# Optimization experiments

Hardware: AMD Instinct MI355X
Metric: run time of the kernel (lower is better)

Reference implementation:

```python
import jax, jax.numpy as jnp
import numpy as np

N_NODES = 100000
NEG_SLOPE = 0.2


def leaky_relu(x):
    return jnp.where(x >= 0, x, NEG_SLOPE * x)


def gat_conv(x, src, dst, W, a_src, a_dst, b, heads, out_ch, concat):
    # x: [N, F_in]; src/dst: [E]; W: [F_in, heads*out_ch]
    n = x.shape[0]
    h = (x @ W).reshape(n, heads, out_ch)                      # [N, H, C]
    s_src = jnp.einsum('nhc,hc->nh', h, a_src)                 # [N, H]
    s_dst = jnp.einsum('nhc,hc->nh', h, a_dst)                 # [N, H]
    e = leaky_relu(s_src[src] + s_dst[dst])                    # [E, H]
    # segment softmax over incoming edges of each dst node
    m = jax.ops.segment_max(e, dst, num_segments=n)            # [N, H]
    m = jnp.where(jnp.isfinite(m), m, 0.0)
    p = jnp.exp(e - m[dst])                                    # [E, H]
    denom = jax.ops.segment_sum(p, dst, num_segments=n)        # [N, H]
    alpha = p / denom[dst]                                     # [E, H]
    out = jax.ops.segment_sum(h[src] * alpha[..., None], dst, num_segments=n)  # [N, H, C]
    if concat:
        out = out.reshape(n, heads * out_ch)
    else:
        out = out.mean(axis=1)
    return out + b


def setup_inputs() -> dict:
    key = jax.random.key(0)
    ks = jax.random.split(key, 10)
    F_in, hidden, heads, n_cls = 128, 32, 8, 40
    n_edges = 1600000
    x = jax.random.normal(ks[0], (N_NODES, F_in), dtype=jnp.float32)
    edge_index = jax.random.randint(ks[1], (2, n_edges), 0, N_NODES, dtype=jnp.int64)
    s = 0.1
    W1 = jax.random.normal(ks[2], (F_in, heads * hidden), dtype=jnp.float32) * s
    att_src1 = jax.random.normal(ks[3], (heads, hidden), dtype=jnp.float32) * s
    att_dst1 = jax.random.normal(ks[4], (heads, hidden), dtype=jnp.float32) * s
    b1 = jnp.zeros((heads * hidden,), dtype=jnp.float32)
    W2 = jax.random.normal(ks[5], (heads * hidden, n_cls), dtype=jnp.float32) * s
    att_src2 = jax.random.normal(ks[6], (1, n_cls), dtype=jnp.float32) * s
    att_dst2 = jax.random.normal(ks[7], (1, n_cls), dtype=jnp.float32) * s
    b2 = jnp.zeros((n_cls,), dtype=jnp.float32)
    return {
        'x': x, 'edge_index': edge_index,
        'W1': W1, 'att_src1': att_src1, 'att_dst1': att_dst1, 'b1': b1,
        'W2': W2, 'att_src2': att_src2, 'att_dst2': att_dst2, 'b2': b2,
    }


def reference(x, edge_index, W1, att_src1, att_dst1, b1, W2, att_src2, att_dst2, b2):
    n = x.shape[0]
    # PyG GATConv default: add self loops
    loop = jnp.arange(n, dtype=edge_index.dtype)
    src = jnp.concatenate([edge_index[0], loop])
    dst = jnp.concatenate([edge_index[1], loop])
    h = gat_conv(x, src, dst, W1, att_src1, att_dst1, b1, heads=8, out_ch=32, concat=True)
    h = jax.nn.relu(h)  # dropout p=0 / eval mode: identity
    out = gat_conv(h, src, dst, W2, att_src2, att_dst2, b2, heads=1, out_ch=40, concat=True)
    return jax.nn.log_softmax(out, axis=1)
```

## Files before the change

### kernel.cpp

```cpp
#include <hip/hip_runtime.h>
#include <hip/hip_bf16.h>
#include <cmath>


typedef unsigned short ushortT;
typedef unsigned int uintT;
typedef unsigned char ucharT;
typedef __attribute__((ext_vector_type(8))) short short8;
typedef __attribute__((ext_vector_type(4))) float float4v;
typedef __attribute__((ext_vector_type(2))) float float2v;

#define LOG2E 1.4426950408889634f

static __device__ __forceinline__ float bflo(uintT u) {
    return __uint_as_float(u << 16);
}
static __device__ __forceinline__ float bfhi(uintT u) {
    return __uint_as_float(u & 0xffff0000u);
}
static __device__ __forceinline__ ushortT f2bf(float f) {
    __hip_bfloat16 h = __float2bfloat16(f);
    return *reinterpret_cast<ushortT*>(&h);
}
static __device__ __forceinline__ uintT pk(float a, float b) {
    return (uintT)f2bf(a) | ((uintT)f2bf(b) << 16);
}
static __device__ __forceinline__ float ub(uintT u, int k) {
    return (float)((u >> (8 * k)) & 0xffu);
}
static __device__ __forceinline__ float lrelu(float e) {
    return 0.6f * e + 0.4f * fabsf(e);
}

#define PREP_BLOCKS 184
#define EPB 4096

__global__ __launch_bounds__(256) void k_prep(const float* __restrict__ W1,
                                              const float* __restrict__ W2,
                                              const float* __restrict__ a1s,
                                              const float* __restrict__ a1d,
                                              ushortT* __restrict__ W1t,
                                              ushortT* __restrict__ W2t) {
    int t = blockIdx.x * 256 + threadIdx.x;
    if (t < 128 * 256) {
        int k = t >> 8, s = t & 255;
        int c = ((s & 15) << 4) | (s >> 4);
        W1t[s * 128 + k] = f2bf(W1[(size_t)k * 256 + c]);
    } else if (t < 128 * 256 + 48 * 256) {
        int q = t - 128 * 256;
        int k = q / 48, c = q - k * 48;
        W2t[c * 256 + k] = (c < 40) ? f2bf(W2[k * 40 + c]) : (ushortT)0;
    } else if (t < 128 * 256 + 48 * 256 + 2048) {
        int q = t - (128 * 256 + 48 * 256);
        int k = q >> 4, j = q & 15;
        int h = j & 7;
        const float* av = ((j < 8) ? a1s : a1d) + h * 32;
        const float* wr = W1 + (size_t)k * 256 + h * 32;
        float s = 0.f;
        #pragma unroll
        for (int c = 0; c < 32; ++c) s += wr[c] * av[c];
        W1t[(256 + j) * 128 + k] = f2bf(s * LOG2E);
    }
}

static __device__ __forceinline__ void dev_gemm1(int slab,
                                                 const float* __restrict__ A,
                                                 const ushortT* __restrict__ Bt,
                                                 ucharT* __restrict__ h1i,
                                                 float* __restrict__ s1cc,
                                                 float* __restrict__ s1d, int M) {
    int lane = threadIdx.x & 63;
    int r0 = slab * 16;
    if (r0 >= M) return;
    int n = lane & 15, q = lane >> 4;
    const float* arow = A + (size_t)(r0 + n) * 128 + q * 8;
    short8 af[4];
    #pragma unroll
    for (int s = 0; s < 4; ++s) {
        float4 v0 = *(const float4*)(arow + s * 32);
        float4 v1 = *(const float4*)(arow + s * 32 + 4);
        short8 a;
        a[0] = (short)f2bf(v0.x); a[1] = (short)f2bf(v0.y);
        a[2] = (short)f2bf(v0.z); a[3] = (short)f2bf(v0.w);
        a[4] = (short)f2bf(v1.x); a[5] = (short)f2bf(v1.y);
        a[6] = (short)f2bf(v1.z); a[7] = (short)f2bf(v1.w);
        af[s] = a;
    }
    float4v acc[17];
    #pragma unroll
    for (int j = 0; j < 17; ++j) acc[j] = (float4v){0.f, 0.f, 0.f, 0.f};
    #pragma unroll
    for (int s = 0; s < 4; ++s) {
        #pragma unroll
        for (int j = 0; j < 17; ++j) {
            short8 b = *(const short8*)(Bt + (size_t)(j * 16 + n) * 128 + s * 32 + q * 8);
            acc[j] = __builtin_amdgcn_mfma_f32_16x16x32_bf16(af[s], b, acc[j], 0, 0, 0);
        }
    }
    float am[4];
    #pragma unroll
    for (int r = 0; r < 4; ++r) {
        float m = 0.f;
        #pragma unroll
        for (int j = 0; j < 16; ++j) m = fmaxf(m, fabsf(acc[j][r]));
        am[r] = m;
    }
    #pragma unroll
    for (int off = 1; off < 16; off <<= 1) {
        #pragma unroll
        for (int r = 0; r < 4; ++r) am[r] = fmaxf(am[r], __shfl_xor(am[r], off, 64));
    }
    #pragma unroll
    for (int r = 0; r < 4; ++r) {
        int row = r0 + q * 4 + r;
        float m = am[r];
        float si = (m > 0.f) ? 127.f / m : 0.f;
        uintT wd[4];
        #pragma unroll
        for (int wq = 0; wq < 4; ++wq) {
            uintT p4 = 0;
            #pragma unroll
            for (int b = 0; b < 4; ++b) {
                int j = wq * 4 + b;
                int qv = (int)rintf(acc[j][r] * si) + 128;
                p4 |= ((uintT)(qv & 0xff)) << (8 * b);
            }
            wd[wq] = p4;
        }
        uint4 o = make_uint4(wd[0], wd[1], wd[2], wd[3]);
        *(uint4*)(h1i + (size_t)row * 256 + n * 16) = o;
        float vv = acc[16][r];
        if (n < 8) {
            *(float2*)(s1cc + ((size_t)row << 4) + n * 2) =
                make_float2(vv, m * (1.f / 127.f));
        } else {
            s1d[(size_t)row * 8 + (n - 8)] = vv;
        }
    }
}

__global__ __launch_bounds__(256) void k_cnt_g1(const int* __restrict__ ei, int E,
                                                int* __restrict__ counts, int nbuck,
                                                const float* __restrict__ A,
                                                const ushortT* __restrict__ Bt,
                                                ucharT* __restrict__ h1i,
                                                float* __restrict__ s1cc,
                                                float* __restrict__ s1d,
                                                int M, int nPrim, int slabBase) {
    if (blockIdx.x >= nPrim) {
        int wave = threadIdx.x >> 6;
        int slab = slabBase + (blockIdx.x - nPrim) * 4 + wave;
        dev_gemm1(slab, A, Bt, h1i, s1cc, s1d, M);
        return;
    }
    __shared__ int h[1024];
    int t = threadIdx.x;
    for (int i = t; i < nbuck; i += 256) h[i] = 0;
    __syncthreads();
    int base = blockIdx.x * EPB;
    #pragma unroll
    for (int r = 0; r < 4; ++r) {
        int i4 = base + (r * 256 + t) * 4;
        if (i4 + 3 < E) {
            int4 d = *(const int4*)(ei + E + i4);
            atomicAdd(&h[d.x >> 7], 1);
            atomicAdd(&h[d.y >> 7], 1);
            atomicAdd(&h[d.z >> 7], 1);
            atomicAdd(&h[d.w >> 7], 1);
        } else {
            for (int j = i4; j < E; ++j) atomicAdd(&h[ei[E + j] >> 7], 1);
        }
    }
    __syncthreads();
    int* crow = counts + (size_t)blockIdx.x * nbuck;
    for (int i = t; i < nbuck; i += 256) crow[i] = h[i];
}

__global__ __launch_bounds__(256) void k_scan_cols(int* __restrict__ counts,
                                                   int* __restrict__ totals,
                                                   int nb1, int nbuck) {
    __shared__ int wsum[4];
    int k = blockIdx.x;
    int t = threadIdx.x, lane = t & 63, wv = t >> 6;
    int e0 = 2 * t, e1 = 2 * t + 1;
    int v0 = (e0 < nb1) ? counts[(size_t)e0 * nbuck + k] : 0;
    int v1 = (e1 < nb1) ? counts[(size_t)e1 * nbuck + k] : 0;
    int s = v0 + v1;
    int incl = s;
    #pragma unroll
    for (int off = 1; off < 64; off <<= 1) {
        int u = __shfl_up(incl, off, 64);
        if (lane >= off) incl += u;
    }
    if (lane == 63) wsum[wv] = incl;
    __syncthreads();
    int add = 0;
    if (wv > 0) add += wsum[0];
    if (wv > 1) add += wsum[1];
    if (wv > 2) add += wsum[2];
    incl += add;
    int excl = incl - s;
    if (e0 < nb1) counts[(size_t)e0 * nbuck + k] = excl;
    if (e1 < nb1) counts[(size_t)e1 * nbuck + k] = excl + v0;
    if (t == 255) totals[k] = incl;
}

__global__ __launch_bounds__(256) void k_place_g1(const int* __restrict__ ei, int E,
                                                  const int* __restrict__ counts,
                                                  const int* __restrict__ totals,
                                                  int* __restrict__ bstart,
                                                  uintT* __restrict__ tmp, int nbuck,
                                                  const float* __restrict__ A,
                                                  const ushortT* __restrict__ Bt,
                                                  ucharT* __restrict__ h1i,
                                                  float* __restrict__ s1cc,
                                                  float* __restrict__ s1d,
                                                  int M, int nPrim, int slabBase) {
    if (blockIdx.x >= nPrim) {
        int wave = threadIdx.x >> 6;
        int slab = slabBase + (blockIdx.x - nPrim) * 4 + wave;
        dev_gemm1(slab, A, Bt, h1i, s1cc, s1d, M);
        return;
    }
    __shared__ int st[1024];
    __shared__ int pos[1024];
    __shared__ int wsum[4];
    int t = threadIdx.x, lane = t & 63, wv = t >> 6;
    int b = blockIdx.x;
    int g[4];
    int s = 0;
    #pragma unroll
    for (int j = 0; j < 4; ++j) {
        int e = 4 * t + j;
        g[j] = (e < nbuck) ? totals[e] : 0;
        s += g[j];
    }
    int incl = s;
    #pragma unroll
    for (int off = 1; off < 64; off <<= 1) {
        int u = __shfl_up(incl, off, 64);
        if (lane >= off) incl += u;
    }
    if (lane == 63) wsum[wv] = incl;
    __syncthreads();
    int add = 0;
    if (wv > 0) add += wsum[0];
    if (wv > 1) add += wsum[1];
    if (wv > 2) add += wsum[2];
    int excl = incl + add - s;
    #pragma unroll
    for (int j = 0; j < 4; ++j) {
        int e = 4 * t + j;
        if (e < nbuck) st[e] = excl;
        excl += g[j];
    }
    __syncthreads();
    const int* crow = counts + (size_t)b * nbuck;
    for (int i = t; i < nbuck; i += 256) {
        int sv = st[i];
        pos[i] = sv + crow[i];
        if (b == 0) bstart[i] = sv;
    }
    __syncthreads();
    int base = b * EPB;
    #pragma unroll
    for (int r = 0; r < 4; ++r) {
        int i4 = base + (r * 256 + t) * 4;
        if (i4 + 3 < E) {
            int4 sv = *(const int4*)(ei + i4);
            int4 dv = *(const int4*)(ei + E + i4);
            int p0 = atomicAdd(&pos[dv.x >> 7], 1);
            tmp[p0] = (uintT)sv.x | (((uintT)dv.x & 127u) << 17);
            int p1 = atomicAdd(&pos[dv.y >> 7], 1);
            tmp[p1] = (uintT)sv.y | (((uintT)dv.y & 127u) << 17);
            int p2 = atomicAdd(&pos[dv.z >> 7], 1);
            tmp[p2] = (uintT)sv.z | (((uintT)dv.z & 127u) << 17);
            int p3 = atomicAdd(&pos[dv.w >> 7], 1);
            tmp[p3] = (uintT)sv.w | (((uintT)dv.w & 127u) << 17);
        } else {
            for (int j = i4; j < E; ++j) {
                int sj = ei[j], dj = ei[E + j];
                int p = atomicAdd(&pos[dj >> 7], 1);
                tmp[p] = (uintT)sj | (((uintT)dj & 127u) << 17);
            }
        }
    }
}

static __device__ __forceinline__ void dev_csr(int k,
                                               const uintT* __restrict__ tmp,
                                               const int* __restrict__ bstart,
                                               const int* __restrict__ totals,
                                               int* __restrict__ rowptr,
                                               int* __restrict__ csr_src,
                                               int N, int* cnt, int* cur,
                                               int* wtot) {
    int t = threadIdx.x;
    int nodeBase = k << 7;
    int nn = N - nodeBase;
    if (nn > 128) nn = 128;
    int myStart = bstart[k];
    int myCount = totals[k];
    int csrBase = myStart + nodeBase;
    if (t < 128) cnt[t] = 0;
    __syncthreads();
    for (int i = t; i < myCount; i += 256) {
        uintT p = tmp[myStart + i];
        atomicAdd(&cnt[p >> 17], 1);
    }
    __syncthreads();
    int dseg = 0, incl = 0;
    if (t < 128) {
        dseg = (t < nn) ? cnt[t] + 1 : 0;
        incl = dseg;
        #pragma unroll
        for (int off = 1; off < 64; off <<= 1) {
            int u = __shfl_up(incl, off, 64);
            if ((t & 63) >= off) incl += u;
        }
        if (t == 63) *wtot = incl;
    }
    __syncthreads();
    if (t < nn) {
        int excl = incl - dseg + ((t >= 64) ? *wtot : 0);
        int rp = csrBase + excl;
        int node = nodeBase + t;
        rowptr[node + 1] = rp + dseg;
        csr_src[rp] = node;
        cur[t] = rp + 1;
    }
    if (k == 0 && t == 0) rowptr[0] = 0;
    __syncthreads();
    for (int i = t; i < myCount; i += 256) {
        uintT p = tmp[myStart + i];
        int ld = p >> 17;
        int q = atomicAdd(&cur[ld], 1);
        csr_src[q] = (int)(p & 0x1FFFFu);
    }
}

__global__ __launch_bounds__(256) void k_csr_g1(const uintT* __restrict__ tmp,
                                                const int* __restrict__ bstart,
                                                const int* __restrict__ totals,
                                                int* __restrict__ rowptr,
                                                int* __restrict__ csr_src,
                                                int N,
                                                const float* __restrict__ A,
                                                const ushortT* __restrict__ Bt,
                                                ucharT* __restrict__ h1i,
                                                float* __restrict__ s1cc,
                                                float* __restrict__ s1d,
                                                int M, int nPrim, int slabBase) {
    __shared__ int cnt[128];
    __shared__ int cur[128];
    __shared__ int wtot;
    if (blockIdx.x >= nPrim) {
        int wave = threadIdx.x >> 6;
        int slab = slabBase + (blockIdx.x - nPrim) * 4 + wave;
        dev_gemm1(slab, A, Bt, h1i, s1cc, s1d, M);
        return;
    }
    dev_csr(blockIdx.x, tmp, bstart, totals, rowptr, csr_src, N, cnt, cur, &wtot);
}

struct Edge1 {
    float2 svc;
    uint4 v;
    int si;
};

static __device__ __forceinline__ void ldi1(Edge1& S, int j, int endm1,
                                            const int* __restrict__ csr_src) {
    int jj = j < endm1 ? j : endm1;
    S.si = csr_src[jj];
}

static __device__ __forceinline__ void ldv1(Edge1& S, int j, int end,
                                            const float2* __restrict__ sc2,
                                            const ucharT* __restrict__ hb, int head) {
    if (j < end) {
        int s = S.si;
        S.svc = sc2[((size_t)s << 3) + head];
        S.v = *(const uint4*)(hb + ((size_t)s << 8));
    }
}

static __device__ __forceinline__ void ac1(const Edge1& S, float sdn,
                                           float2v* A, float& l, float& sps) {
    float p = exp2f(lrelu(S.svc.x + sdn));
    l += p;
    float ps = p * S.svc.y;
    sps += ps;
    float2v p2 = {ps, ps};
    uintT w;
    w = S.v.x;
    A[0] += p2 * (float2v){ub(w, 0), ub(w, 1)};
    A[1] += p2 * (float2v){ub(w, 2), ub(w, 3)};
    w = S.v.y;
    A[2] += p2 * (float2v){ub(w, 0), ub(w, 1)};
    A[3] += p2 * (float2v){ub(w, 2), ub(w, 3)};
    w = S.v.z;
    A[4] += p2 * (float2v){ub(w, 0), ub(w, 1)};
    A[5] += p2 * (float2v){ub(w, 2), ub(w, 3)};
    w = S.v.w;
    A[6] += p2 * (float2v){ub(w, 0), ub(w, 1)};
    A[7] += p2 * (float2v){ub(w, 2), ub(w, 3)};
}

static __device__ __forceinline__ void dev_agg1(int n,
                                                const ucharT* __restrict__ h1i,
                                                const float* __restrict__ s1cc,
                                                const float* __restrict__ s1d,
                                                const int* __restrict__ rowptr,
                                                const int* __restrict__ csr_src,
                                                const float* __restrict__ b1,
                                                ushortT* __restrict__ out1) {
    int lane = threadIdx.x & 63;
    int g = lane >> 4;
    int cl = lane & 15;
    int head = cl >> 1;
    int beg = rowptr[n], end = rowptr[n + 1];
    float sdn = s1d[(size_t)n * 8 + head];
    const ucharT* hb = h1i + cl * 16;
    const float2* sc2 = (const float2*)s1cc;
    float2v A[8];
    #pragma unroll
    for (int k = 0; k < 8; ++k) A[k] = (float2v){0.f, 0.f};
    float l = 0.f, sps = 0.f;
    int i0 = beg + g;
    if (i0 < end) {
        int endm1 = end - 1;
        Edge1 S0, S1, S2;
        S0.svc = S1.svc = S2.svc = make_float2(0.f, 0.f);
        S0.v = S1.v = S2.v = make_uint4(0u, 0u, 0u, 0u);
        ldi1(S0, i0, endm1, csr_src);
        ldi1(S1, i0 + 4, endm1, csr_src);
        ldi1(S2, i0 + 8, endm1, csr_src);
        ldv1(S0, i0, end, sc2, hb, head);
        ldv1(S1, i0 + 4, end, sc2, hb, head);
        ldv1(S2, i0 + 8, end, sc2, hb, head);
        ldi1(S0, i0 + 12, endm1, csr_src);
        ldi1(S1, i0 + 16, endm1, csr_src);
        ldi1(S2, i0 + 20, endm1, csr_src);
        for (int idx = i0; idx < end; idx += 12) {
            ac1(S0, sdn, A, l, sps);
            ldv1(S0, idx + 12, end, sc2, hb, head);
            ldi1(S0, idx + 24, endm1, csr_src);
            if (idx + 4 < end) {
                ac1(S1, sdn, A, l, sps);
                ldv1(S1, idx + 16, end, sc2, hb, head);
                ldi1(S1, idx + 28, endm1, csr_src);
            }
            if (idx + 8 < end) {
                ac1(S2, sdn, A, l, sps);
                ldv1(S2, idx + 20, end, sc2, hb, head);
                ldi1(S2, idx + 32, endm1, csr_src);
            }
        }
    }
    #pragma unroll
    for (int off = 16; off < 64; off <<= 1) {
        l += __shfl_xor(l, off, 64);
        sps += __shfl_xor(sps, off, 64);
        #pragma unroll
        for (int k = 0; k < 8; ++k) {
            A[k].x += __shfl_xor(A[k].x, off, 64);
            A[k].y += __shfl_xor(A[k].y, off, 64);
        }
    }
    if (g == 0) {
        float inv = 1.f / l;
        float adj = 128.f * sps;
        const float4 bb0 = *(const float4*)(b1 + cl * 16);
        const float4 bb1 = *(const float4*)(b1 + cl * 16 + 4);
        const float4 bb2 = *(const float4*)(b1 + cl * 16 + 8);
        const float4 bb3 = *(const float4*)(b1 + cl * 16 + 12);
        float bbf[16] = {bb0.x, bb0.y, bb0.z, bb0.w, bb1.x, bb1.y, bb1.z, bb1.w,
                         bb2.x, bb2.y, bb2.z, bb2.w, bb3.x, bb3.y, bb3.z, bb3.w};
        uintT o[8];
        #pragma unroll
        for (int k = 0; k < 8; ++k) {
            float x0 = fmaxf((A[k].x - adj) * inv + bbf[2 * k], 0.f);
            float x1 = fmaxf((A[k].y - adj) * inv + bbf[2 * k + 1], 0.f);
            o[k] = pk(x0, x1);
        }
        *(uint4*)(out1 + (size_t)n * 256 + cl * 16) =
            make_uint4(o[0], o[1], o[2], o[3]);
        *(uint4*)(out1 + (size_t)n * 256 + cl * 16 + 8) =
            make_uint4(o[4], o[5], o[6], o[7]);
    }
}

__global__ __launch_bounds__(256) void k_csr_agg1(const uintT* __restrict__ tmp,
                                                  const int* __restrict__ bstart,
                                                  const int* __restrict__ totals,
                                                  int* __restrict__ rowptr,
                                                  int* __restrict__ csr_src,
                                                  int N, int halfB, int nP4,
                                                  const ucharT* __restrict__ h1i,
                                                  const float* __restrict__ s1cc,
                                                  const float* __restrict__ s1d,
                                                  const float* __restrict__ b1,
                                                  ushortT* __restrict__ out1, int H) {
    __shared__ int cnt[128];
    __shared__ int cur[128];
    __shared__ int wtot;
    if (blockIdx.x < nP4) {
        dev_csr(halfB + blockIdx.x, tmp, bstart, totals, rowptr, csr_src, N,
                cnt, cur, &wtot);
        return;
    }
    int n = (blockIdx.x - nP4) * 4 + (threadIdx.x >> 6);
    if (n >= H) return;
    dev_agg1(n, h1i, s1cc, s1d, rowptr, csr_src, b1, out1);
}

__global__ __launch_bounds__(256) void k_agg1(const ucharT* __restrict__ h1i,
                                              const float* __restrict__ s1cc,
                                              const float* __restrict__ s1d,
                                              const int* __restrict__ rowptr,
                                              const int* __restrict__ csr_src,
                                              const float* __restrict__ b1,
                                              ushortT* __restrict__ out1,
                                              int base, int N) {
    int n = base + blockIdx.x * 4 + (threadIdx.x >> 6);
    if (n >= N) return;
    dev_agg1(n, h1i, s1cc, s1d, rowptr, csr_src, b1, out1);
}

__global__ __launch_bounds__(256) void k_gemm2(const ushortT* __restrict__ X,
                                               const ushortT* __restrict__ Bt,
                                               const float* __restrict__ a2s,
                                               const float* __restrict__ a2d,
                                               ushortT* __restrict__ H2,
                                               float* __restrict__ s2d, int M) {
    int lane = threadIdx.x & 63, wave = threadIdx.x >> 6;
    int slab = blockIdx.x * 4 + wave;
    int r0 = slab * 16;
    if (r0 >= M) return;
    int n = lane & 15, q = lane >> 4;
    const ushortT* xrow = X + (size_t)(r0 + n) * 256 + q * 8;
    float4v acc[3];
    #pragma unroll
    for (int j = 0; j < 3; ++j) acc[j] = (float4v){0.f, 0.f, 0.f, 0.f};
    #pragma unroll
    for (int s = 0; s < 8; ++s) {
        short8 a = *(const short8*)(xrow + s * 32);
        #pragma unroll
        for (int j = 0; j < 3; ++j) {
            short8 b = *(const short8*)(Bt + (size_t)(j * 16 + n) * 256 + s * 32 + q * 8);
            acc[j] = __builtin_amdgcn_mfma_f32_16x16x32_bf16(a, b, acc[j], 0, 0, 0);
        }
    }
    float asv[3], adv[3];
    #pragma unroll
    for (int j = 0; j < 3; ++j) {
        int col = j * 16 + n;
        asv[j] = (col < 40) ? a2s[col] * LOG2E : 0.f;
        adv[j] = (col < 40) ? a2d[col] * LOG2E : 0.f;
    }
    float us[4], ud[4];
    #pragma unroll
    for (int r = 0; r < 4; ++r) {
        us[r] = acc[0][r] * asv[0] + acc[1][r] * asv[1] + acc[2][r] * asv[2];
        ud[r] = acc[0][r] * adv[0] + acc[1][r] * adv[1] + acc[2][r] * adv[2];
    }
    #pragma unroll
    for (int off = 1; off < 16; off <<= 1) {
        #pragma unroll
        for (int r = 0; r < 4; ++r) {
            us[r] += __shfl_xor(us[r], off, 64);
            ud[r] += __shfl_xor(ud[r], off, 64);
        }
    }
    #pragma unroll
    for (int j = 0; j < 3; ++j) {
        int col = j * 16 + n;
        if (col < 40) {
            #pragma unroll
            for (int r = 0; r < 4; ++r)
                H2[(size_t)(r0 + q * 4 + r) * 48 + col] = f2bf(acc[j][r]);
        }
    }
    if (n == 0) {
        #pragma unroll
        for (int r = 0; r < 4; ++r) {
            int row = r0 + q * 4 + r;
            *(float*)(H2 + (size_t)row * 48 + 40) = us[r];
            s2d[row] = ud[r];
        }
    }
}

struct Edge2 {
    float sv;
    uint2 v;
    int si;
};

static __device__ __forceinline__ void ldi2(Edge2& S, int j, int endm1,
                                            const int* __restrict__ csr_src) {
    int jj = j < endm1 ? j : endm1;
    S.si = csr_src[jj];
}

static __device__ __forceinline__ void ldv2(Edge2& S, int j, int end,
                                            const ushortT* __restrict__ h2, int cl) {
    if (j < end) {
        int s = S.si;
        const ushortT* hr = h2 + (size_t)s * 48;
        S.v = *(const uint2*)(hr + cl * 4);
        S.sv = *(const float*)(hr + 40);
    }
}

static __device__ __forceinline__ void ac2(const Edge2& S, float sdn,
                                           float2v& A01, float2v& A23, float& l) {
    float p = exp2f(lrelu(S.sv + sdn));
    l += p;
    float2v p2 = {p, p};
    A01 += p2 * (float2v){bflo(S.v.x), bfhi(S.v.x)};
    A23 += p2 * (float2v){bflo(S.v.y), bfhi(S.v.y)};
}

__global__ __launch_bounds__(256) void k_agg2lsm(const ushortT* __restrict__ h2,
                                                 const float* __restrict__ sd,
                                                 const int* __restrict__ rowptr,
                                                 const int* __restrict__ csr_src,
                                                 const float* __restrict__ b2,
                                                 float* __restrict__ out, int N) {
    int lane = threadIdx.x & 63;
    int wid = threadIdx.x >> 6;
    int n = blockIdx.x * 4 + wid;
    if (n >= N) return;
    int el = lane / 10;
    int cl = lane - el * 10;
    int beg = rowptr[n], end = rowptr[n + 1];
    float sdn = sd[n];
    float2v A01 = (float2v){0.f, 0.f}, A23 = (float2v){0.f, 0.f};
    float l = 0.f;
    if (el < 6) {
        int i0 = beg + el;
        if (i0 < end) {
            int endm1 = end - 1;
            Edge2 S0, S1, S2;
            S0.sv = S1.sv = S2.sv = 0.f;
            S0.v = S1.v = S2.v = make_uint2(0u, 0u);
            ldi2(S0, i0, endm1, csr_src);
            ldi2(S1, i0 + 6, endm1, csr_src);
            ldi2(S2, i0 + 12, endm1, csr_src);
            ldv2(S0, i0, end, h2, cl);
            ldv2(S1, i0 + 6, end, h2, cl);
            ldv2(S2, i0 + 12, end, h2, cl);
            ldi2(S0, i0 + 18, endm1, csr_src);
            ldi2(S1, i0 + 24, endm1, csr_src);
            ldi2(S2, i0 + 30, endm1, csr_src);
            for (int idx = i0; idx < end; idx += 18) {
                ac2(S0, sdn, A01, A23, l);
                ldv2(S0, idx + 18, end, h2, cl);
                ldi2(S0, idx + 36, endm1, csr_src);
                if (idx + 6 < end) {
                    ac2(S1, sdn, A01, A23, l);
                    ldv2(S1, idx + 24, end, h2, cl);
                    ldi2(S1, idx + 42, endm1, csr_src);
                }
                if (idx + 12 < end) {
                    ac2(S2, sdn, A01, A23, l);
                    ldv2(S2, idx + 30, end, h2, cl);
                    ldi2(S2, idx + 48, endm1, csr_src);
                }
            }
        }
    }
    float a0 = A01.x, a1 = A01.y, a2 = A23.x, a3 = A23.y;
    float t0 = 0.f, t1 = 0.f, t2 = 0.f, t3 = 0.f, lt = 0.f;
    #pragma unroll
    for (int k = 0; k < 6; ++k) {
        int sl = cl + 10 * k;
        t0 += __shfl(a0, sl, 64);
        t1 += __shfl(a1, sl, 64);
        t2 += __shfl(a2, sl, 64);
        t3 += __shfl(a3, sl, 64);
        if (cl == 0) lt += __shfl(l, sl, 64);
    }
    lt = __shfl(lt, 0, 64);
    float inv = 1.f / lt;
    float o0 = t0 * inv + b2[cl * 4 + 0];
    float o1 = t1 * inv + b2[cl * 4 + 1];
    float o2 = t2 * inv + b2[cl * 4 + 2];
    float o3 = t3 * inv + b2[cl * 4 + 3];
    float lm = (lane < 10) ? fmaxf(fmaxf(o0, o1), fmaxf(o2, o3)) : -INFINITY;
    #pragma unroll
    for (int off = 32; off; off >>= 1) lm = fmaxf(lm, __shfl_xor(lm, off, 64));
    float le = (lane < 10)
        ? __expf(o0 - lm) + __expf(o1 - lm) + __expf(o2 - lm) + __expf(o3 - lm)
        : 0.f;
    #pragma unroll
    for (int off = 32; off; off >>= 1) le += __shfl_xor(le, off, 64);
    float ls = lm + logf(le);
    if (lane < 10) {
        float4 w = make_float4(o0 - ls, o1 - ls, o2 - ls, o3 - ls);
        *(float4*)(out + (size_t)n * 40 + cl * 4) = w;
    }
}

extern "C" void kernel_launch(void* const* d_in, const int* in_sizes, int n_in,
                              void* d_out, int out_size, void* d_ws, size_t ws_size,
                              hipStream_t stream) {
    const float* x   = (const float*)d_in[0];
    const int*   ei  = (const int*)d_in[1];
    const float* W1  = (const float*)d_in[2];
    const float* a1s = (const float*)d_in[3];
    const float* a1d = (const float*)d_in[4];
    const float* b1  = (const float*)d_in[5];
    const float* W2  = (const float*)d_in[6];
    const float* a2s = (const float*)d_in[7];
    const float* a2d = (const float*)d_in[8];
    const float* b2  = (const float*)d_in[9];
    float* out = (float*)d_out;

    const int N = in_sizes[0] / 128;
    const int E = in_sizes[1] / 2;
    const int ET = E + N;
    const int NBUCK = (N + 127) >> 7;
    const int NB1 = (E + EPB - 1) / EPB;

    char* w = (char*)d_ws;
    ucharT* h1i = (ucharT*)w;
    ushortT* out1b = (ushortT*)(w + (size_t)N * 256);
    int* i_row = (int*)(w + (size_t)N * 768);
    float* s1cc = (float*)(w + (size_t)N * 768 + ((size_t)N + 16) * 4);
    float* s1d = s1cc + (size_t)N * 16;
    int* i_cnt = (int*)(s1d + (size_t)N * 8);
    int* i_tot = i_cnt + (size_t)NB1 * NBUCK;
    int* i_bst = i_tot + NBUCK + 2;
    uintT* i_tmp = (uintT*)(i_bst + NBUCK + 2);
    int* i_csr = (int*)(i_tmp + E);
    ushortT* W1t = (ushortT*)(i_csr + ET);
    ushortT* W2t = W1t + 272 * 128;
    ushortT* h2b = (ushortT*)s1cc;
    float* s2d = (float*)i_cnt;

    const int nb4 = (N + 3) / 4;
    const int nbG = (N / 16 + 3) / 4;
    const int CH  = (nbG + 2) / 3;
    const int halfB = NBUCK >> 1;
    const int H = halfB << 7;
    const int nP4b = NBUCK - halfB;

    k_prep<<<PREP_BLOCKS, 256, 0, stream>>>(W1, W2, a1s, a1d, W1t, W2t);
    k_cnt_g1<<<NB1 + CH, 256, 0, stream>>>(ei, E, i_cnt, NBUCK,
                                           x, W1t, h1i, s1cc, s1d,
                                           N, NB1, 0);
    k_scan_cols<<<NBUCK, 256, 0, stream>>>(i_cnt, i_tot, NB1, NBUCK);
    k_place_g1<<<NB1 + CH, 256, 0, stream>>>(ei, E, i_cnt, i_tot, i_bst, i_tmp, NBUCK,
                                             x, W1t, h1i, s1cc, s1d,
                                             N, NB1, CH * 4);
    k_csr_g1<<<halfB + CH, 256, 0, stream>>>(i_tmp, i_bst, i_tot, i_row, i_csr, N,
                                             x, W1t, h1i, s1cc, s1d,
                                             N, halfB, CH * 8);
    k_csr_agg1<<<nP4b + H / 4, 256, 0, stream>>>(i_tmp, i_bst, i_tot, i_row, i_csr,
                                                 N, halfB, nP4b,
                                                 h1i, s1cc, s1d, b1, out1b, H);
    k_agg1<<<(N - H + 3) / 4, 256, 0, stream>>>(h1i, s1cc, s1d, i_row, i_csr, b1,
                                                out1b, H, N);

    k_gemm2<<<nbG, 256, 0, stream>>>(out1b, W2t, a2s, a2d, h2b, s2d, N);
    k_agg2lsm<<<nb4, 256, 0, stream>>>(h2b, s2d, i_row, i_csr, b2, out, N);
}
```

Measured before the change: 407.1 us.

## Aggregate two nodes per wave in layer-1 attention and simplify layer-2 reduction

Layer-1 aggregation now gives each 64-lane wave two destination nodes, with 32 lanes (2 edge groups of 16) per node instead of 4 groups over one node. This halves the cross-group shuffle reduction and the wasted lanes on low-degree nodes, at the cost of less edge-level parallelism and shorter prefetch distance per node. The layer-2 aggregation reduction is also restructured: a fold of lanes 30+ into lanes 0-29 followed by a 3-way gather replaces the 6-step shuffle loop.

```diff
diff --git a/kernel.cpp b/kernel.cpp
--- a/kernel.cpp
+++ b/kernel.cpp
@@ -407,20 +407,28 @@
     A[7] += p2 * (float2v){ub(w, 2), ub(w, 3)};
 }
 
-static __device__ __forceinline__ void dev_agg1(int n,
-                                                const ucharT* __restrict__ h1i,
-                                                const float* __restrict__ s1cc,
-                                                const float* __restrict__ s1d,
-                                                const int* __restrict__ rowptr,
-                                                const int* __restrict__ csr_src,
-                                                const float* __restrict__ b1,
-                                                ushortT* __restrict__ out1) {
+static __device__ __forceinline__ void dev_agg1_pair(int n0, int NN,
+                                                     const ucharT* __restrict__ h1i,
+                                                     const float* __restrict__ s1cc,
+                                                     const float* __restrict__ s1d,
+                                                     const int* __restrict__ rowptr,
+                                                     const int* __restrict__ csr_src,
+                                                     const float* __restrict__ b1,
+                                                     ushortT* __restrict__ out1) {
     int lane = threadIdx.x & 63;
-    int g = lane >> 4;
-    int cl = lane & 15;
+    int half = lane >> 5;
+    int n = n0 + half;
+    bool act = n < NN;
+    int l32 = lane & 31;
+    int g = l32 >> 4;
+    int cl = l32 & 15;
     int head = cl >> 1;
-    int beg = rowptr[n], end = rowptr[n + 1];
-    float sdn = s1d[(size_t)n * 8 + head];
+    int beg = 0, end = 0;
+    if (act) {
+        beg = rowptr[n];
+        end = rowptr[n + 1];
+    }
+    float sdn = act ? s1d[(size_t)n * 8 + head] : 0.f;
     const ucharT* hb = h1i + cl * 16;
     const float2* sc2 = (const float2*)s1cc;
     float2v A[8];
@@ -434,41 +442,38 @@
         S0.svc = S1.svc = S2.svc = make_float2(0.f, 0.f);
         S0.v = S1.v = S2.v = make_uint4(0u, 0u, 0u, 0u);
         ldi1(S0, i0, endm1, csr_src);
-        ldi1(S1, i0 + 4, endm1, csr_src);
-        ldi1(S2, i0 + 8, endm1, csr_src);
+        ldi1(S1, i0 + 2, endm1, csr_src);
+        ldi1(S2, i0 + 4, endm1, csr_src);
         ldv1(S0, i0, end, sc2, hb, head);
-        ldv1(S1, i0 + 4, end, sc2, hb, head);
-        ldv1(S2, i0 + 8, end, sc2, hb, head);
-        ldi1(S0, i0 + 12, endm1, csr_src);
-        ldi1(S1, i0 + 16, endm1, csr_src);
-        ldi1(S2, i0 + 20, endm1, csr_src);
-        for (int idx = i0; idx < end; idx += 12) {
+        ldv1(S1, i0 + 2, end, sc2, hb, head);
+        ldv1(S2, i0 + 4, end, sc2, hb, head);
+        ldi1(S0, i0 + 6, endm1, csr_src);
+        ldi1(S1, i0 + 8, endm1, csr_src);
+        ldi1(S2, i0 + 10, endm1, csr_src);
+        for (int idx = i0; idx < end; idx += 6) {
             ac1(S0, sdn, A, l, sps);
-            ldv1(S0, idx + 12, end, sc2, hb, head);
-            ldi1(S0, idx + 24, endm1, csr_src);
+            ldv1(S0, idx + 6, end, sc2, hb, head);
+            ldi1(S0, idx + 12, endm1, csr_src);
+            if (idx + 2 < end) {
+                ac1(S1, sdn, A, l, sps);
+                ldv1(S1, idx + 8, end, sc2, hb, head);
+                ldi1(S1, idx + 14, endm1, csr_src);
+            }
             if (idx + 4 < end) {
-                ac1(S1, sdn, A, l, sps);
-                ldv1(S1, idx + 16, end, sc2, hb, head);
-                ldi1(S1, idx + 28, endm1, csr_src);
+                ac1(S2, sdn, A, l, sps);
+                ldv1(S2, idx + 10, end, sc2, hb, head);
+                ldi1(S2, idx + 16, endm1, csr_src);
             }
-            if (idx + 8 < end) {
-                ac1(S2, sdn, A, l, sps);
-                ldv1(S2, idx + 20, end, sc2, hb, head);
-                ldi1(S2, idx + 32, endm1, csr_src);
-            }
-        }
-    }
-    #pragma unroll
-    for (int off = 16; off < 64; off <<= 1) {
-        l += __shfl_xor(l, off, 64);
-        sps += __shfl_xor(sps, off, 64);
-        #pragma unroll
-        for (int k = 0; k < 8; ++k) {
-            A[k].x += __shfl_xor(A[k].x, off, 64);
-            A[k].y += __shfl_xor(A[k].y, off, 64);
-        }
-    }
-    if (g == 0) {
+        }
+    }
+    l += __shfl_xor(l, 16, 64);
+    sps += __shfl_xor(sps, 16, 64);
+    #pragma unroll
+    for (int k = 0; k < 8; ++k) {
+        A[k].x += __shfl_xor(A[k].x, 16, 64);
+        A[k].y += __shfl_xor(A[k].y, 16, 64);
+    }
+    if (g == 0 && act) {
         float inv = 1.f / l;
         float adj = 128.f * sps;
         const float4 bb0 = *(const float4*)(b1 + cl * 16);
@@ -510,9 +515,9 @@
                 cnt, cur, &wtot);
         return;
     }
-    int n = (blockIdx.x - nP4) * 4 + (threadIdx.x >> 6);
-    if (n >= H) return;
-    dev_agg1(n, h1i, s1cc, s1d, rowptr, csr_src, b1, out1);
+    int n0 = (blockIdx.x - nP4) * 8 + (threadIdx.x >> 6) * 2;
+    if (n0 >= H) return;
+    dev_agg1_pair(n0, H, h1i, s1cc, s1d, rowptr, csr_src, b1, out1);
 }
 
 __global__ __launch_bounds__(256) void k_agg1(const ucharT* __restrict__ h1i,
@@ -523,9 +528,9 @@
                                               const float* __restrict__ b1,
                                               ushortT* __restrict__ out1,
                                               int base, int N) {
-    int n = base + blockIdx.x * 4 + (threadIdx.x >> 6);
-    if (n >= N) return;
-    dev_agg1(n, h1i, s1cc, s1d, rowptr, csr_src, b1, out1);
+    int n0 = base + blockIdx.x * 8 + (threadIdx.x >> 6) * 2;
+    if (n0 >= N) return;
+    dev_agg1_pair(n0, N, h1i, s1cc, s1d, rowptr, csr_src, b1, out1);
 }
 
 __global__ __launch_bounds__(256) void k_gemm2(const ushortT* __restrict__ X,
@@ -673,17 +678,21 @@
         }
     }
     float a0 = A01.x, a1 = A01.y, a2 = A23.x, a3 = A23.y;
-    float t0 = 0.f, t1 = 0.f, t2 = 0.f, t3 = 0.f, lt = 0.f;
-    #pragma unroll
-    for (int k = 0; k < 6; ++k) {
-        int sl = cl + 10 * k;
-        t0 += __shfl(a0, sl, 64);
-        t1 += __shfl(a1, sl, 64);
-        t2 += __shfl(a2, sl, 64);
-        t3 += __shfl(a3, sl, 64);
-        if (cl == 0) lt += __shfl(l, sl, 64);
-    }
-    lt = __shfl(lt, 0, 64);
+    int src = lane + 30;
+    if (src > 63) src = 63;
+    bool f = (el < 3);
+    float u;
+    u = __shfl(a0, src, 64); if (f) a0 += u;
+    u = __shfl(a1, src, 64); if (f) a1 += u;
+    u = __shfl(a2, src, 64); if (f) a2 += u;
+    u = __shfl(a3, src, 64); if (f) a3 += u;
+    u = __shfl(l, src, 64);  if (f) l += u;
+    int s1 = cl + 10, s2 = cl + 20;
+    float t0 = a0 + __shfl(a0, s1, 64) + __shfl(a0, s2, 64);
+    float t1 = a1 + __shfl(a1, s1, 64) + __shfl(a1, s2, 64);
+    float t2 = a2 + __shfl(a2, s1, 64) + __shfl(a2, s2, 64);
+    float t3 = a3 + __shfl(a3, s1, 64) + __shfl(a3, s2, 64);
+    float lt = l + __shfl(l, s1, 64) + __shfl(l, s2, 64);
     float inv = 1.f / lt;
     float o0 = t0 * inv + b2[cl * 4 + 0];
     float o1 = t1 * inv + b2[cl * 4 + 1];
@@ -747,6 +756,8 @@
     const int halfB = NBUCK >> 1;
     const int H = halfB << 7;
     const int nP4b = NBUCK - halfB;
+    const int nAgg1a = (H + 7) / 8;
+    const int nAgg1b = (N - H + 7) / 8;
 
     k_prep<<<PREP_BLOCKS, 256, 0, stream>>>(W1, W2, a1s, a1d, W1t, W2t);
     k_cnt_g1<<<NB1 + CH, 256, 0, stream>>>(ei, E, i_cnt, NBUCK,
@@ -759,11 +770,11 @@
     k_csr_g1<<<halfB + CH, 256, 0, stream>>>(i_tmp, i_bst, i_tot, i_row, i_csr, N,
                                              x, W1t, h1i, s1cc, s1d,
                                              N, halfB, CH * 8);
-    k_csr_agg1<<<nP4b + H / 4, 256, 0, stream>>>(i_tmp, i_bst, i_tot, i_row, i_csr,
-                                                 N, halfB, nP4b,
-                                                 h1i, s1cc, s1d, b1, out1b, H);
-    k_agg1<<<(N - H + 3) / 4, 256, 0, stream>>>(h1i, s1cc, s1d, i_row, i_csr, b1,
-                                                out1b, H, N);
+    k_csr_agg1<<<nP4b + nAgg1a, 256, 0, stream>>>(i_tmp, i_bst, i_tot, i_row, i_csr,
+                                                  N, halfB, nP4b,
+                                                  h1i, s1cc, s1d, b1, out1b, H);
+    k_agg1<<<nAgg1b, 256, 0, stream>>>(h1i, s1cc, s1d, i_row, i_csr, b1,
+                                       out1b, H, N);
 
     k_gemm2<<<nbG, 256, 0, stream>>>(out1b, W2t, a2s, a2d, h2b, s2d, N);
     k_agg2lsm<<<nb4, 256, 0, stream>>>(h2b, s2d, i_row, i_csr, b2, out, N);
```

Measured after the change: 398.8 us. 1.02x faster.
